# Kernel tuning notes

Hardware: AMD Instinct MI355X
Metric: run time of the kernel (lower is better)

Reference implementation:

```python
import jax, jax.numpy as jnp
import numpy as np
import math

EMBED_DIM = 1024
NUM_HEADS = 16
HEAD_DIM = EMBED_DIM // NUM_HEADS
B, S = 2, 2048


def setup_inputs() -> dict:
    key = jax.random.key(0)
    ks = jax.random.split(key, 5)
    scale = 1.0 / math.sqrt(EMBED_DIM)
    x = jax.random.normal(ks[0], (B, S, EMBED_DIM), dtype=jnp.float32)
    W_q = jax.random.normal(ks[1], (EMBED_DIM, EMBED_DIM), dtype=jnp.float32) * scale
    W_k = jax.random.normal(ks[2], (EMBED_DIM, EMBED_DIM), dtype=jnp.float32) * scale
    W_v = jax.random.normal(ks[3], (EMBED_DIM, EMBED_DIM), dtype=jnp.float32) * scale
    W_o = jax.random.normal(ks[4], (EMBED_DIM, EMBED_DIM), dtype=jnp.float32) * scale
    # causal mask: True = masked out (matches torch masked_fill semantics)
    mask = jnp.triu(jnp.ones((S, S), dtype=bool), k=1)
    return {"x": x, "mask": mask, "W_q": W_q, "W_k": W_k, "W_v": W_v, "W_o": W_o}


def _split_heads(x):
    b, s, _ = x.shape
    return x.reshape(b, s, NUM_HEADS, HEAD_DIM).transpose(0, 2, 1, 3)  # [b,h,s,hd]


def reference(x, mask, W_q, W_k, W_v, W_o):
    # torch nn.Linear(bias=False): y = x @ W.T
    Q = _split_heads(x @ W_q.T)
    K = _split_heads(x @ W_k.T)
    V = _split_heads(x @ W_v.T)
    scale = 1.0 / math.sqrt(HEAD_DIM)
    scores = jnp.einsum("bhqd,bhkd->bhqk", Q, K) * scale  # [b,h,s,s]
    scores = jnp.where(mask[None, None, :, :], -jnp.inf, scores)
    weights = jax.nn.softmax(scores, axis=-1)
    out = jnp.einsum("bhqk,bhkd->bhqd", weights, V)
    out = out.transpose(0, 2, 1, 3).reshape(x.shape[0], x.shape[1], EMBED_DIM)
    return out @ W_o.T
```

## Files before the change

kernel.cpp:

```cpp
#include <hip/hip_runtime.h>
#include <hip/hip_bf16.h>

typedef short bf16x8 __attribute__((ext_vector_type(8)));
typedef unsigned short u16x8 __attribute__((ext_vector_type(8)));
typedef unsigned short u16x4 __attribute__((ext_vector_type(4)));
typedef float f32x4 __attribute__((ext_vector_type(4)));

typedef unsigned int __attribute__((address_space(1))) gu32;
typedef unsigned int __attribute__((address_space(3))) lu32;

#define MFMA16(a, b, c) __builtin_amdgcn_mfma_f32_16x16x32_bf16((a), (b), (c), 0, 0, 0)

constexpr int SEQ = 2048;
constexpr int NH = 16;
constexpr int NTOK = 2 * SEQ;

__device__ __forceinline__ float bf2f(unsigned short u) {
  union { unsigned int i; float f; } v; v.i = ((unsigned int)u) << 16; return v.f;
}
__device__ __forceinline__ unsigned short f2bf(float f) {
  __hip_bfloat16 h = __float2bfloat16(f);
  return __builtin_bit_cast(unsigned short, h);
}
__device__ __forceinline__ unsigned int pkbf_trunc(float hi, float lo) {
  return __builtin_amdgcn_perm(__builtin_bit_cast(unsigned int, hi),
                               __builtin_bit_cast(unsigned int, lo), 0x07060302u);
}
__device__ __forceinline__ u16x8 cvt8(const float* __restrict__ p) {
  f32x4 a = *(const f32x4*)p;
  f32x4 b = *(const f32x4*)(p + 4);
  u16x8 r;
#pragma unroll
  for (int j = 0; j < 4; j++) { r[j] = f2bf(a[j]); r[4 + j] = f2bf(b[j]); }
  return r;
}

__global__ __launch_bounds__(256) void cvt_all(
    const float* __restrict__ x, const float* __restrict__ wq, const float* __restrict__ wk,
    const float* __restrict__ wv, const float* __restrict__ wo,
    unsigned short* __restrict__ Xb, unsigned short* __restrict__ Wb) {
  const size_t XN = (size_t)NTOK * 1024;
  const size_t TOT = XN + (size_t)4 * 1024 * 1024;
  for (size_t i = ((size_t)blockIdx.x * 256 + threadIdx.x) * 8; i < TOT;
       i += (size_t)gridDim.x * 256 * 8) {
    if (i < XN) {
      *(u16x8*)(Xb + i) = cvt8(x + i);
    } else {
      const size_t j = i - XN;
      const int w = (int)(j >> 20);
      const float* src = (w == 0) ? wq : (w == 1) ? wk : (w == 2) ? wv : wo;
      *(u16x8*)(Wb + j) = cvt8(src + (j & (((size_t)1 << 20) - 1)));
    }
  }
}

template <int ROWS, int NWAVE>
__device__ __forceinline__ void stage_glds(const unsigned short* __restrict__ gbase,
                                           int rstride,
                                           unsigned short* __restrict__ lds,
                                           int wid, int lane) {
  constexpr int ISS = ROWS * 8 / (NWAVE * 64);
#pragma unroll
  for (int t = 0; t < ISS; ++t) {
    const int slot = (wid * ISS + t) * 64 + lane;
    const int row = slot >> 3;
    const int c8 = (slot & 7) ^ (row & 7);
    const unsigned short* gp = gbase + (size_t)row * rstride + c8 * 8;
    unsigned short* lp = lds + (size_t)(wid * ISS + t) * 512;
    __builtin_amdgcn_global_load_lds((const gu32*)gp, (lu32*)lp, 16, 0, 0);
  }
}

__device__ __forceinline__ bf16x8 frag_ld(const unsigned short* __restrict__ lds, int row, int c8) {
  const int slot = row * 8 + (c8 ^ (row & 7));
  return *(const bf16x8*)(lds + slot * 8);
}

#define SBAR do { __builtin_amdgcn_sched_barrier(0); \
                  asm volatile("s_barrier" ::: "memory"); \
                  __builtin_amdgcn_sched_barrier(0); } while (0)

__global__ __launch_bounds__(256) void gemm_op_bk128(
    const unsigned short* __restrict__ A,
    const unsigned short* __restrict__ B,
    float* __restrict__ C) {
  constexpr int K = 1024;
  constexpr int MI = 4, NI = 2;
  __shared__ __align__(16) unsigned short As[2][128 * 64];
  __shared__ __align__(16) unsigned short Bs[2][64 * 64];

  const int tid = threadIdx.x;
  const int wid = tid >> 6;
  const int lane = tid & 63;
  const int quad = lane >> 4;
  const int c16 = lane & 15;
  const int wrow = wid >> 1, wcol = wid & 1;

  const int m0 = blockIdx.x * 128;
  const int n0 = blockIdx.y * 64;

  f32x4 acc[MI][NI];
#pragma unroll
  for (int i = 0; i < MI; i++)
#pragma unroll
    for (int j = 0; j < NI; j++) acc[i][j] = f32x4{0.f, 0.f, 0.f, 0.f};

  for (int kb = 0; kb < K; kb += 128) {
    __syncthreads();
    stage_glds<128, 4>(A + (size_t)m0 * K + kb, K, As[0], wid, lane);
    stage_glds<128, 4>(A + (size_t)m0 * K + kb + 64, K, As[1], wid, lane);
    stage_glds<64, 4>(B + (size_t)n0 * K + kb, K, Bs[0], wid, lane);
    stage_glds<64, 4>(B + (size_t)n0 * K + kb + 64, K, Bs[1], wid, lane);
    __syncthreads();
#pragma unroll
    for (int ks = 0; ks < 4; ++ks) {
      const unsigned short* Asr = As[ks >> 1];
      const unsigned short* Bsr = Bs[ks >> 1];
      const int c8 = (ks & 1) * 4 + quad;
      bf16x8 af[MI], bfr[NI];
#pragma unroll
      for (int i = 0; i < MI; i++)
        af[i] = frag_ld(Asr, wrow * 64 + i * 16 + c16, c8);
#pragma unroll
      for (int j = 0; j < NI; j++)
        bfr[j] = frag_ld(Bsr, wcol * 32 + j * 16 + c16, c8);
#pragma unroll
      for (int i = 0; i < MI; i++)
#pragma unroll
        for (int j = 0; j < NI; j++) acc[i][j] = MFMA16(af[i], bfr[j], acc[i][j]);
    }
  }

#pragma unroll
  for (int i = 0; i < MI; i++) {
#pragma unroll
    for (int j = 0; j < NI; j++) {
      const int row = m0 + wrow * 64 + i * 16 + quad * 4;
      const int col = n0 + wcol * 32 + j * 16 + c16;
#pragma unroll
      for (int r = 0; r < 4; r++)
        C[(size_t)(row + r) * 1024 + col] = acc[i][j][r];
    }
  }
}

__global__ __launch_bounds__(512) void gemm_4ph_w192(
    const unsigned short* __restrict__ A,
    const unsigned short* __restrict__ B,
    unsigned short* __restrict__ C) {
  constexpr int K = 1024;
  __shared__ __align__(16) unsigned short As[2][256 * 64];
  __shared__ __align__(16) unsigned short Bs[2][192 * 64];

  const int tid = threadIdx.x;
  const int wid = tid >> 6, lane = tid & 63;
  const int quad = lane >> 4, c16 = lane & 15;
  const int wr = wid >> 2;
  const int wc = wid & 3;

  const int bid = blockIdx.x;
  const int swz = (bid & 7) * 32 + (bid >> 3);
  const int m0 = (swz >> 4) * 256;
  const int n0 = (swz & 15) * 192;

  const unsigned short* Abase = A + (size_t)m0 * K;
  const unsigned short* Bbase = B + (size_t)n0 * K;

  f32x4 acc[8][3];
#pragma unroll
  for (int i = 0; i < 8; i++)
#pragma unroll
    for (int j = 0; j < 3; j++) acc[i][j] = f32x4{0.f, 0.f, 0.f, 0.f};

  bf16x8 af[4][2];
  bf16x8 bf0[3];
  bf16x8 bf1[3];

  auto lda8 = [&](const unsigned short* asb, int mo) {
#pragma unroll
    for (int mi = 0; mi < 4; mi++)
#pragma unroll
      for (int ks = 0; ks < 2; ks++)
        af[mi][ks] = frag_ld(asb, wr * 128 + (mo + mi) * 16 + c16, ks * 4 + quad);
  };
  auto ldb6 = [&](const unsigned short* bsb) {
#pragma unroll
    for (int ni = 0; ni < 3; ni++) {
      bf0[ni] = frag_ld(bsb, wc * 48 + ni * 16 + c16, quad);
      bf1[ni] = frag_ld(bsb, wc * 48 + ni * 16 + c16, 4 + quad);
    }
  };
  auto mm24 = [&](int mo) {
    __builtin_amdgcn_s_setprio(1);
#pragma unroll
    for (int mi = 0; mi < 4; mi++)
#pragma unroll
      for (int ni = 0; ni < 3; ni++) {
        acc[mo + mi][ni] = MFMA16(af[mi][0], bf0[ni], acc[mo + mi][ni]);
        acc[mo + mi][ni] = MFMA16(af[mi][1], bf1[ni], acc[mo + mi][ni]);
      }
    __builtin_amdgcn_s_setprio(0);
  };

  stage_glds<192, 8>(Bbase, K, Bs[0], wid, lane);
  stage_glds<128, 8>(Abase, K, As[0], wid, lane);
  stage_glds<128, 8>(Abase + (size_t)128 * K, K, As[0] + 8192, wid, lane);
  stage_glds<192, 8>(Bbase + 64, K, Bs[1], wid, lane);
  asm volatile("s_waitcnt vmcnt(3)" ::: "memory");
  SBAR;

  for (int i = 0; i < 7; ++i) {
    const int t = 2 * i;
    const int kb1 = (t + 1) * 64, kb2 = (t + 2) * 64, kb3 = (t + 3) * 64;
    lda8(As[0], 0); ldb6(Bs[0]);
    stage_glds<128, 8>(Abase + kb1, K, As[1], wid, lane);
    stage_glds<128, 8>(Abase + (size_t)128 * K + kb1, K, As[1] + 8192, wid, lane);
    mm24(0); SBAR;
    lda8(As[0], 4);
    stage_glds<192, 8>(Bbase + kb2, K, Bs[0], wid, lane);
    asm volatile("s_waitcnt vmcnt(3)" ::: "memory");
    mm24(4); SBAR;
    lda8(As[1], 0); ldb6(Bs[1]);
    stage_glds<128, 8>(Abase + kb2, K, As[0], wid, lane);
    stage_glds<128, 8>(Abase + (size_t)128 * K + kb2, K, As[0] + 8192, wid, lane);
    mm24(0); SBAR;
    lda8(As[1], 4);
    stage_glds<192, 8>(Bbase + kb3, K, Bs[1], wid, lane);
    asm volatile("s_waitcnt vmcnt(3)" ::: "memory");
    mm24(4); SBAR;
  }

  {
    const int kb1 = 15 * 64;
    lda8(As[0], 0); ldb6(Bs[0]);
    stage_glds<128, 8>(Abase + kb1, K, As[1], wid, lane);
    stage_glds<128, 8>(Abase + (size_t)128 * K + kb1, K, As[1] + 8192, wid, lane);
    mm24(0); SBAR;
    lda8(As[0], 4);
    asm volatile("s_waitcnt vmcnt(0)" ::: "memory");
    mm24(4); SBAR;
    lda8(As[1], 0); ldb6(Bs[1]);
    mm24(0); SBAR;
    lda8(As[1], 4);
    mm24(4);
  }

#pragma unroll
  for (int mi = 0; mi < 8; mi++) {
#pragma unroll
    for (int ni = 0; ni < 3; ni++) {
      const int row = m0 + wr * 128 + mi * 16 + quad * 4;
      const int col = n0 + wc * 48 + ni * 16 + c16;
#pragma unroll
      for (int r = 0; r < 4; r++)
        C[(size_t)(row + r) * 3072 + col] = f2bf(acc[mi][ni][r]);
    }
  }
}

__device__ __forceinline__ int vt_idx(int d, int kv) {
  int ck = kv >> 3;
  int s = ((d >> 3) ^ d) & 7;
  return d * 64 + ((ck ^ s) << 3) + (kv & 7);
}

struct AttnShared {
  unsigned short Kt[2][64 * 64];
  unsigned short Vt[2][64 * 64];
  unsigned short Pt[4][16 * 64];
};

__global__ __launch_bounds__(256) void attn_kernel(
    const unsigned short* __restrict__ QKV,
    unsigned short* __restrict__ Oa) {
  __shared__ AttnShared sh;
  const int h = blockIdx.x;
  const int b = blockIdx.y;
  const int t = 31 - blockIdx.z;
  const int tid = threadIdx.x;
  const int wid = tid >> 6, lane = tid & 63;
  const int quad = lane >> 4, c16 = lane & 15;
  const size_t tokbase = (size_t)b * SEQ;
  const int q0 = t * 64;
  const int nkv = t + 1;

  const unsigned short* qp = QKV + (tokbase + q0 + wid * 16 + c16) * 3072 + h * 64;
  bf16x8 qf[2];
#pragma unroll
  for (int ks = 0; ks < 2; ++ks) {
    u16x8 u = *(const u16x8*)(qp + ks * 32 + quad * 8);
    bf16x8 tq;
#pragma unroll
    for (int j = 0; j < 8; j++) tq[j] = (short)f2bf(0.1803368801f * bf2f(u[j]));
    qf[ks] = tq;
  }

  const unsigned short* kbase = QKV + tokbase * 3072 + 1024 + h * 64;
  const unsigned short* vbase = QKV + tokbase * 3072 + 2048 + h * 64;
  const int vkv = (tid >> 4) * 4;
  const int vd = (tid & 15) * 4;

  f32x4 o[4];
  float lacc = 0.f;
#pragma unroll
  for (int nt = 0; nt < 4; nt++) o[nt] = f32x4{0.f, 0.f, 0.f, 0.f};
  unsigned short* PtW = sh.Pt[wid];
  const int pt_sub = (quad & 1) * 4;
  const int pt_c8h = quad >> 1;

  stage_glds<64, 4>(kbase, 3072, sh.Kt[0], wid, lane);
  u16x4 vr[4];
#pragma unroll
  for (int i = 0; i < 4; i++)
    vr[i] = *(const u16x4*)(vbase + (size_t)(vkv + i) * 3072 + vd);
#pragma unroll
  for (int dd = 0; dd < 4; ++dd) {
    uint2 w;
    w.x = (unsigned int)vr[0][dd] | ((unsigned int)vr[1][dd] << 16);
    w.y = (unsigned int)vr[2][dd] | ((unsigned int)vr[3][dd] << 16);
    *(uint2*)&sh.Vt[0][vt_idx(vd + dd, vkv)] = w;
  }

  for (int kt = 0; kt < nkv; ++kt) {
    const int buf = kt & 1;
    __syncthreads();

    const bool pf = (kt + 1 < nkv);
    if (pf) {
      const size_t nofs = (size_t)(kt + 1) * 64;
      stage_glds<64, 4>(kbase + nofs * 3072, 3072, sh.Kt[buf ^ 1], wid, lane);
#pragma unroll
      for (int i = 0; i < 4; i++)
        vr[i] = *(const u16x4*)(vbase + (nofs + vkv + i) * 3072 + vd);
    }

    const unsigned short* KtB = sh.Kt[buf];
    f32x4 st[4];
    __builtin_amdgcn_s_setprio(1);
#pragma unroll
    for (int nt = 0; nt < 4; ++nt) {
      f32x4 a = f32x4{-16.f, -16.f, -16.f, -16.f};
      a = MFMA16(frag_ld(KtB, nt * 16 + c16, quad), qf[0], a);
      a = MFMA16(frag_ld(KtB, nt * 16 + c16, 4 + quad), qf[1], a);
      st[nt] = a;
    }
    __builtin_amdgcn_s_setprio(0);
    if (kt == nkv - 1) {
      const int kv0 = kt * 64;
      const int qg = q0 + wid * 16 + c16;
#pragma unroll
      for (int nt = 0; nt < 4; nt++)
#pragma unroll
        for (int r = 0; r < 4; r++) {
          int kg = kv0 + nt * 16 + quad * 4 + r;
          if (kg > qg) st[nt][r] = -1e30f;
        }
    }

#pragma unroll
    for (int nt = 0; nt < 4; nt++) {
      float p0 = __builtin_amdgcn_exp2f(st[nt][0]);
      float p1 = __builtin_amdgcn_exp2f(st[nt][1]);
      float p2 = __builtin_amdgcn_exp2f(st[nt][2]);
      float p3 = __builtin_amdgcn_exp2f(st[nt][3]);
      lacc += (p0 + p1) + (p2 + p3);
      uint2 w;
      w.x = pkbf_trunc(p1, p0);
      w.y = pkbf_trunc(p3, p2);
      const int c8w = 2 * nt + pt_c8h;
      const int slot = c16 * 8 + (c8w ^ (c16 & 7));
      *(uint2*)&PtW[slot * 8 + pt_sub] = w;
    }

    if (pf) {
#pragma unroll
      for (int dd = 0; dd < 4; ++dd) {
        uint2 w;
        w.x = (unsigned int)vr[0][dd] | ((unsigned int)vr[1][dd] << 16);
        w.y = (unsigned int)vr[2][dd] | ((unsigned int)vr[3][dd] << 16);
        *(uint2*)&sh.Vt[buf ^ 1][vt_idx(vd + dd, vkv)] = w;
      }
    }

    const unsigned short* VtB = sh.Vt[buf];
    __builtin_amdgcn_s_setprio(1);
#pragma unroll
    for (int ks = 0; ks < 2; ++ks) {
      bf16x8 pfrag = frag_ld(PtW, c16, ks * 4 + quad);
#pragma unroll
      for (int nt2 = 0; nt2 < 4; ++nt2) {
        bf16x8 vf = *(const bf16x8*)&VtB[vt_idx(nt2 * 16 + c16, ks * 32 + quad * 8)];
        o[nt2] = MFMA16(vf, pfrag, o[nt2]);
      }
    }
    __builtin_amdgcn_s_setprio(0);
  }

  lacc += __shfl_xor(lacc, 16);
  lacc += __shfl_xor(lacc, 32);
  const float linv = 1.f / lacc;
  const size_t row = tokbase + q0 + wid * 16 + c16;
#pragma unroll
  for (int nt2 = 0; nt2 < 4; nt2++) {
    uint2 w;
    w.x = (unsigned int)f2bf(o[nt2][0] * linv) | ((unsigned int)f2bf(o[nt2][1] * linv) << 16);
    w.y = (unsigned int)f2bf(o[nt2][2] * linv) | ((unsigned int)f2bf(o[nt2][3] * linv) << 16);
    *(uint2*)&Oa[row * 1024 + h * 64 + nt2 * 16 + quad * 4] = w;
  }
}

template <int BM, int BN, int LDC, bool AF32, bool CF32>
__global__ __launch_bounds__(256) void gemm_bt(
    const void* __restrict__ Av, const float* __restrict__ W0, const float* __restrict__ W1,
    const float* __restrict__ W2, void* __restrict__ Cv) {
  constexpr int K = 1024;
  constexpr int LDS_LD = 72;
  constexpr int MI = BM / 32, NI = BN / 32;
  __shared__ __align__(16) unsigned short As[BM][LDS_LD];
  __shared__ __align__(16) unsigned short Bs[BN][LDS_LD];
  const int tid = threadIdx.x, wid = tid >> 6, lane = tid & 63;
  const int quad = lane >> 4, c16 = lane & 15;
  const int wrow = wid >> 1, wcol = wid & 1;
  const float* W = (blockIdx.z == 0) ? W0 : (blockIdx.z == 1 ? W1 : W2);
  const int m0 = blockIdx.y * BM, n0 = blockIdx.x * BN, cofs = blockIdx.z * 1024;
  f32x4 acc[MI][NI];
#pragma unroll
  for (int i = 0; i < MI; i++)
#pragma unroll
    for (int j = 0; j < NI; j++) acc[i][j] = f32x4{0.f, 0.f, 0.f, 0.f};
  for (int kb = 0; kb < K; kb += 64) {
    __syncthreads();
#pragma unroll
    for (int c = tid; c < BM * 8; c += 256) {
      int row = c >> 3, c8 = c & 7;
      if constexpr (AF32)
        *(u16x8*)&As[row][c8 * 8] = cvt8((const float*)Av + (size_t)(m0 + row) * K + kb + c8 * 8);
      else
        *(u16x8*)&As[row][c8 * 8] = *(const u16x8*)((const unsigned short*)Av + (size_t)(m0 + row) * K + kb + c8 * 8);
    }
#pragma unroll
    for (int c = tid; c < BN * 8; c += 256) {
      int row = c >> 3, c8 = c & 7;
      *(u16x8*)&Bs[row][c8 * 8] = cvt8(W + (size_t)(n0 + row) * K + kb + c8 * 8);
    }
    __syncthreads();
#pragma unroll
    for (int ks = 0; ks < 2; ++ks) {
      bf16x8 af[MI], bfr[NI];
#pragma unroll
      for (int i = 0; i < MI; i++)
        af[i] = *(const bf16x8*)&As[wrow * (BM / 2) + i * 16 + c16][ks * 32 + quad * 8];
#pragma unroll
      for (int j = 0; j < NI; j++)
        bfr[j] = *(const bf16x8*)&Bs[wcol * (BN / 2) + j * 16 + c16][ks * 32 + quad * 8];
#pragma unroll
      for (int i = 0; i < MI; i++)
#pragma unroll
        for (int j = 0; j < NI; j++) acc[i][j] = MFMA16(af[i], bfr[j], acc[i][j]);
    }
  }
#pragma unroll
  for (int i = 0; i < MI; i++)
#pragma unroll
    for (int j = 0; j < NI; j++) {
      int row = m0 + wrow * (BM / 2) + i * 16 + quad * 4;
      int col = n0 + wcol * (BN / 2) + j * 16 + c16 + cofs;
#pragma unroll
      for (int r = 0; r < 4; r++) {
        if constexpr (CF32) ((float*)Cv)[(size_t)(row + r) * LDC + col] = acc[i][j][r];
        else ((unsigned short*)Cv)[(size_t)(row + r) * LDC + col] = f2bf(acc[i][j][r]);
      }
    }
}

extern "C" void kernel_launch(void* const* d_in, const int* in_sizes, int n_in,
                              void* d_out, int out_size, void* d_ws, size_t ws_size,
                              hipStream_t stream) {
  const float* x = (const float*)d_in[0];
  const float* Wq = (const float*)d_in[2];
  const float* Wk = (const float*)d_in[3];
  const float* Wv = (const float*)d_in[4];
  const float* Wo = (const float*)d_in[5];
  float* out = (float*)d_out;

  unsigned short* QKV = (unsigned short*)d_ws;
  unsigned short* Wb = QKV + (size_t)NTOK * 3072;
  unsigned short* Xb = Wb + (size_t)4 * 1024 * 1024;
  unsigned short* AT = Xb;

  if (ws_size >= (size_t)40 * 1024 * 1024) {
    cvt_all<<<dim3(2048), 256, 0, stream>>>(x, Wq, Wk, Wv, Wo, Xb, Wb);
    gemm_4ph_w192<<<dim3(256), 512, 0, stream>>>(Xb, Wb, QKV);
    attn_kernel<<<dim3(NH, 2, 32), 256, 0, stream>>>(QKV, AT);
    gemm_op_bk128<<<dim3(32, 16), 256, 0, stream>>>(
        AT, Wb + (size_t)3 * 1024 * 1024, out);
  } else {
    unsigned short* QKV2 = (unsigned short*)d_ws;
    unsigned short* AT2 = QKV2 + (size_t)NTOK * 3072;
    gemm_bt<128, 128, 3072, true, false><<<dim3(8, 32, 3), 256, 0, stream>>>(x, Wq, Wk, Wv, QKV2);
    attn_kernel<<<dim3(NH, 2, 32), 256, 0, stream>>>(QKV2, AT2);
    gemm_bt<64, 64, 1024, false, true><<<dim3(16, 64, 1), 256, 0, stream>>>(AT2, Wo, Wo, Wo, out);
  }
}
```

Before: 171.1 us.

## Triple-buffer B tiles in QKV GEMM to use one barrier per k-step

The fused QKV projection GEMM moves from a four-phase schedule with a barrier after every half-tile of MFMA work to a two-phase loop with a single barrier per 64-wide k-step. The B tile gets a third LDS buffer so it can be prefetched two k-steps ahead while A stays double-buffered. The aim is to cut workgroup synchronisation stalls and let global-to-LDS loads overlap more MFMA work. The cost is about 24 KB more LDS per block, which could lower occupancy, and less fine-grained interleaving of loads with compute.

```diff
diff --git a/kernel.cpp b/kernel.cpp
--- a/kernel.cpp
+++ b/kernel.cpp
@@ -144,13 +144,13 @@
   }
 }
 
-__global__ __launch_bounds__(512) void gemm_4ph_w192(
+__global__ __launch_bounds__(512) void gemm_2ph_w192(
     const unsigned short* __restrict__ A,
     const unsigned short* __restrict__ B,
     unsigned short* __restrict__ C) {
   constexpr int K = 1024;
   __shared__ __align__(16) unsigned short As[2][256 * 64];
-  __shared__ __align__(16) unsigned short Bs[2][192 * 64];
+  __shared__ __align__(16) unsigned short Bs[3][192 * 64];
 
   const int tid = threadIdx.x;
   const int wid = tid >> 6, lane = tid & 63;
@@ -209,38 +209,40 @@
   asm volatile("s_waitcnt vmcnt(3)" ::: "memory");
   SBAR;
 
-  for (int i = 0; i < 7; ++i) {
-    const int t = 2 * i;
-    const int kb1 = (t + 1) * 64, kb2 = (t + 2) * 64, kb3 = (t + 3) * 64;
-    lda8(As[0], 0); ldb6(Bs[0]);
+#pragma unroll 2
+  for (int t = 0; t < 14; ++t) {
+    const int abuf = t & 1;
+    const unsigned short* AsR = As[abuf];
+    unsigned short* AsW = As[abuf ^ 1];
+    const unsigned short* BsR = Bs[t % 3];
+    unsigned short* BsW = Bs[(t + 2) % 3];
+    const int kb1 = (t + 1) * 64, kb2 = (t + 2) * 64;
+
+    lda8(AsR, 0); ldb6(BsR);
+    stage_glds<128, 8>(Abase + kb1, K, AsW, wid, lane);
+    stage_glds<128, 8>(Abase + (size_t)128 * K + kb1, K, AsW + 8192, wid, lane);
+    stage_glds<192, 8>(Bbase + kb2, K, BsW, wid, lane);
+    mm24(0);
+    lda8(AsR, 4);
+    mm24(4);
+    asm volatile("s_waitcnt vmcnt(3)" ::: "memory");
+    SBAR;
+  }
+
+  {
+    const int kb1 = 15 * 64;
+    lda8(As[0], 0); ldb6(Bs[2]);
     stage_glds<128, 8>(Abase + kb1, K, As[1], wid, lane);
     stage_glds<128, 8>(Abase + (size_t)128 * K + kb1, K, As[1] + 8192, wid, lane);
-    mm24(0); SBAR;
+    mm24(0);
     lda8(As[0], 4);
-    stage_glds<192, 8>(Bbase + kb2, K, Bs[0], wid, lane);
-    asm volatile("s_waitcnt vmcnt(3)" ::: "memory");
-    mm24(4); SBAR;
-    lda8(As[1], 0); ldb6(Bs[1]);
-    stage_glds<128, 8>(Abase + kb2, K, As[0], wid, lane);
-    stage_glds<128, 8>(Abase + (size_t)128 * K + kb2, K, As[0] + 8192, wid, lane);
-    mm24(0); SBAR;
-    lda8(As[1], 4);
-    stage_glds<192, 8>(Bbase + kb3, K, Bs[1], wid, lane);
-    asm volatile("s_waitcnt vmcnt(3)" ::: "memory");
-    mm24(4); SBAR;
-  }
-
+    mm24(4);
+    asm volatile("s_waitcnt vmcnt(0)" ::: "memory");
+    SBAR;
+  }
   {
-    const int kb1 = 15 * 64;
-    lda8(As[0], 0); ldb6(Bs[0]);
-    stage_glds<128, 8>(Abase + kb1, K, As[1], wid, lane);
-    stage_glds<128, 8>(Abase + (size_t)128 * K + kb1, K, As[1] + 8192, wid, lane);
-    mm24(0); SBAR;
-    lda8(As[0], 4);
-    asm volatile("s_waitcnt vmcnt(0)" ::: "memory");
-    mm24(4); SBAR;
-    lda8(As[1], 0); ldb6(Bs[1]);
-    mm24(0); SBAR;
+    lda8(As[1], 0); ldb6(Bs[0]);
+    mm24(0);
     lda8(As[1], 4);
     mm24(4);
   }
@@ -490,7 +492,7 @@
 
   if (ws_size >= (size_t)40 * 1024 * 1024) {
     cvt_all<<<dim3(2048), 256, 0, stream>>>(x, Wq, Wk, Wv, Wo, Xb, Wb);
-    gemm_4ph_w192<<<dim3(256), 512, 0, stream>>>(Xb, Wb, QKV);
+    gemm_2ph_w192<<<dim3(256), 512, 0, stream>>>(Xb, Wb, QKV);
     attn_kernel<<<dim3(NH, 2, 32), 256, 0, stream>>>(QKV, AT);
     gemm_op_bk128<<<dim3(32, 16), 256, 0, stream>>>(
         AT, Wb + (size_t)3 * 1024 * 1024, out);
```

Result: no change. 168.5 us (-1.5%).
